# Kernel optimization log

Measured on AMD Instinct MI355X. Metric: run time of the kernel, lower is better.

Reference implementation:

```python
import jax, jax.numpy as jnp
import numpy as np

D_MODEL = 1024
N_HEADS = 16
HEAD_DIM = D_MODEL // N_HEADS  # 64; note: scores use full d_model dots but sqrt(head_dim) scale
WINDOW = 256
B, S = 4, 4096


def _window_starts(seq_len, ws):
    # replicate the torch loop: half-stride overlapping windows
    stride = ws // 2
    starts = []
    for i in range(0, seq_len, stride):
        end = min(i + ws, seq_len)
        start = max(0, end - ws)
        starts.append(start)
        if end == seq_len:
            break
    return np.asarray(starts, dtype=np.int32)


def setup_inputs() -> dict:
    key = jax.random.key(0)
    ks = jax.random.split(key, 9)
    sc = 0.02
    x = jax.random.normal(ks[0], (B, S, D_MODEL), dtype=jnp.float32)
    Wq = jax.random.normal(ks[1], (D_MODEL, D_MODEL), dtype=jnp.float32) * sc
    bq = jnp.zeros((D_MODEL,), jnp.float32)
    Wk = jax.random.normal(ks[2], (D_MODEL, D_MODEL), dtype=jnp.float32) * sc
    bk = jnp.zeros((D_MODEL,), jnp.float32)
    Wv = jax.random.normal(ks[3], (D_MODEL, D_MODEL), dtype=jnp.float32) * sc
    bv = jnp.zeros((D_MODEL,), jnp.float32)
    Wo = jax.random.normal(ks[4], (D_MODEL, D_MODEL), dtype=jnp.float32) * sc
    bo = jnp.zeros((D_MODEL,), jnp.float32)
    return {"x": x, "Wq": Wq, "bq": bq, "Wk": Wk, "bk": bk,
            "Wv": Wv, "bv": bv, "Wo": Wo, "bo": bo}


def reference(x, Wq, bq, Wk, bk, Wv, bv, Wo, bo):
    Bsz, seq, dm = x.shape
    q = x @ Wq + bq  # [B,S,D] (heads are re-flattened in the windowed path anyway)
    k = x @ Wk + bk
    v = x @ Wv + bv

    starts = _window_starts(seq, WINDOW)            # [W]
    idx = starts[:, None] + np.arange(WINDOW)[None]  # [W, ws] static indices
    idx_j = jnp.asarray(idx)

    qw = q[:, idx_j, :]  # [B, W, ws, D]
    kw = k[:, idx_j, :]
    vw = v[:, idx_j, :]

    scale = 1.0 / np.sqrt(HEAD_DIM).astype(np.float32)
    scores = jnp.einsum('bwid,bwjd->bwij', qw, kw) * scale  # full-d_model dots
    attn = jax.nn.softmax(scores, axis=-1)
    ow = jnp.einsum('bwij,bwjd->bwid', attn, vw)  # [B, W, ws, D]

    flat_idx = idx_j.reshape(-1)  # [W*ws]
    out = jnp.zeros_like(q).at[:, flat_idx, :].add(ow.reshape(Bsz, -1, dm))
    counts = jnp.zeros((seq,), jnp.float32).at[flat_idx].add(1.0)
    out = out / counts[None, :, None]  # overlap-add average

    return out @ Wo + bo
```

## Files before the change

### kernel.cpp

```cpp
#include <hip/hip_runtime.h>
#include <hip/hip_bf16.h>

typedef unsigned short u16;
typedef short bf16x8 __attribute__((ext_vector_type(8)));
typedef float f32x4 __attribute__((ext_vector_type(4)));
typedef float f32x16 __attribute__((ext_vector_type(16)));

#define DM     1024
#define SEQ    4096
#define NBATCH 4
#define NWIN   31
#define NTOK   16384

__device__ __forceinline__ u16 f2b(float f) {
  union { float f; unsigned u; } x; x.f = f;
  unsigned r = (x.u + 0x7fffu + ((x.u >> 16) & 1u)) >> 16;
  return (u16)r;
}
__device__ __forceinline__ float b2f(u16 v) {
  union { unsigned u; float f; } x; x.u = ((unsigned)v) << 16; return x.f;
}
__device__ __forceinline__ void gload_lds16(const u16* g, u16* l) {
  __builtin_amdgcn_global_load_lds(
      (const __attribute__((address_space(1))) void*)g,
      (__attribute__((address_space(3))) void*)l, 16, 0, 0);
}

__global__ __launch_bounds__(256) void k_convert(const float* __restrict__ in,
                                                 u16* __restrict__ out, int n4) {
  int i = blockIdx.x * 256 + threadIdx.x;
  if (i >= n4) return;
  float4 v = ((const float4*)in)[i];
  ushort4 o; o.x = f2b(v.x); o.y = f2b(v.y); o.z = f2b(v.z); o.w = f2b(v.w);
  ((ushort4*)out)[i] = o;
}

__global__ __launch_bounds__(256) void k_transpose4(const float* __restrict__ W0,
                                                    const float* __restrict__ W1,
                                                    const float* __restrict__ W2,
                                                    const float* __restrict__ W3,
                                                    u16* __restrict__ Wt) {
  __shared__ float tile[32][33];
  int z = blockIdx.z;
  const float* W = (z == 0) ? W0 : (z == 1) ? W1 : (z == 2) ? W2 : W3;
  u16* dst = Wt + (size_t)z * DM * DM;
  int n0 = blockIdx.x * 32, k0 = blockIdx.y * 32;
  int tx = threadIdx.x, ty = threadIdx.y;
  #pragma unroll
  for (int i = ty; i < 32; i += 8) tile[i][tx] = W[(size_t)(k0 + i) * DM + n0 + tx];
  __syncthreads();
  #pragma unroll
  for (int i = ty; i < 32; i += 8) dst[(size_t)(n0 + i) * DM + k0 + tx] = f2b(tile[tx][i]);
}

__global__ __launch_bounds__(256) void k_catbias(const float* __restrict__ bq,
                                                 const float* __restrict__ bk,
                                                 const float* __restrict__ bv,
                                                 float* __restrict__ o) {
  int i = blockIdx.x * 256 + threadIdx.x;
  if (i >= 3 * DM) return;
  float v = (i < DM) ? bq[i] : (i < 2 * DM) ? bk[i - DM] : bv[i - 2 * DM];
  o[i] = v;
}

__global__ __launch_bounds__(256, 4) void k_gemm(const u16* __restrict__ A, const u16* __restrict__ Bt,
                                                 const float* __restrict__ bias,
                                                 float* __restrict__ Cf,
                                                 u16* __restrict__ Cb, int ldc,
                                                 u16* __restrict__ Ct, int csplit,
                                                 int M, int N, int K) {
  __shared__ u16 As[128 * 64];
  __shared__ u16 Bs[128 * 64];
  const int tid = threadIdx.x;
  const int wv = tid >> 6, lane = tid & 63;
  const int l31 = lane & 31, hl = lane >> 5;
  const int lr8 = lane >> 3;
  const int lc8 = (((lane & 7) ^ (lr8 & 7)) * 8);
  const int m0 = blockIdx.y * 128, n0 = blockIdx.x * 128;
  const int wm = (wv >> 1) * 64, wn = (wv & 1) * 64;
  const int k7 = l31 & 7;
  f32x16 acc[2][2];
  #pragma unroll
  for (int a = 0; a < 2; ++a)
    #pragma unroll
    for (int b = 0; b < 2; ++b)
      #pragma unroll
      for (int r = 0; r < 16; ++r) acc[a][b][r] = 0.f;

  for (int kk = 0; kk < K; kk += 64) {
    #pragma unroll
    for (int j = 0; j < 4; ++j) {
      int e = wv * 4 + j;
      gload_lds16(A + (size_t)(m0 + e * 8 + lr8) * K + kk + lc8, As + e * 512);
    }
    #pragma unroll
    for (int j = 0; j < 4; ++j) {
      int e = wv * 4 + j;
      gload_lds16(Bt + (size_t)(n0 + e * 8 + lr8) * K + kk + lc8, Bs + e * 512);
    }
    __syncthreads();
    #pragma unroll
    for (int s = 0; s < 4; ++s) {
      const int ch = ((2 * s + hl) ^ k7) * 8;
      bf16x8 af[2], bfr[2];
      #pragma unroll
      for (int t = 0; t < 2; ++t) af[t]  = *(const bf16x8*)&As[(wm + t * 32 + l31) * 64 + ch];
      #pragma unroll
      for (int t = 0; t < 2; ++t) bfr[t] = *(const bf16x8*)&Bs[(wn + t * 32 + l31) * 64 + ch];
      #pragma unroll
      for (int mt = 0; mt < 2; ++mt)
        #pragma unroll
        for (int nt = 0; nt < 2; ++nt)
          acc[mt][nt] = __builtin_amdgcn_mfma_f32_32x32x16_bf16(af[mt], bfr[nt], acc[mt][nt], 0, 0, 0);
    }
    __syncthreads();
  }
  #pragma unroll
  for (int mt = 0; mt < 2; ++mt) {
    #pragma unroll
    for (int nt = 0; nt < 2; ++nt) {
      int col = n0 + wn + nt * 32 + l31;
      float bv = bias[col];
      #pragma unroll
      for (int g = 0; g < 4; ++g) {
        int row = m0 + wm + mt * 32 + g * 8 + hl * 4;
        if (Cf) {
          #pragma unroll
          for (int r = 0; r < 4; ++r)
            Cf[(size_t)(row + r) * N + col] = acc[mt][nt][g * 4 + r] + bv;
        } else if (col < csplit) {
          #pragma unroll
          for (int r = 0; r < 4; ++r)
            Cb[(size_t)(row + r) * ldc + col] = f2b(acc[mt][nt][g * 4 + r] + bv);
        } else {
          ushort4 o;
          o.x = f2b(acc[mt][nt][g * 4 + 0] + bv); o.y = f2b(acc[mt][nt][g * 4 + 1] + bv);
          o.z = f2b(acc[mt][nt][g * 4 + 2] + bv); o.w = f2b(acc[mt][nt][g * 4 + 3] + bv);
          *(ushort4*)&Ct[(size_t)(col - csplit) * M + row] = o;
        }
      }
    }
  }
}

#define PSTR 264
#define LDQ  2048
__global__ __launch_bounds__(256) void k_attn(const u16* __restrict__ QKb, const u16* __restrict__ Vt,
                                              u16* __restrict__ oA, u16* __restrict__ oB) {
  __shared__ u16 stage[10240];
  __shared__ u16 Pbuf[64 * PSTR];
  u16* Qs = stage;
  u16* Ks = stage + 2048;
  u16* Vs = stage;

  const int tid = threadIdx.x;
  const int wv = tid >> 6, lane = tid & 63;
  const int quad = lane >> 4, l16 = lane & 15;
  const int lr = lane >> 2;
  const int lc = (((lane & 3) ^ ((lr >> 1) & 3)) * 8);
  const int k3 = (l16 >> 1) & 3;
  const int qt = blockIdx.x >> 1, h = blockIdx.x & 1;
  const int w = blockIdx.y, b = blockIdx.z;
  const int s0 = w * 128;
  const size_t base2 = (size_t)b * SEQ * LDQ;
  const size_t base  = (size_t)b * SEQ * DM;
  const size_t btok  = (size_t)b * SEQ;
  const int qrow0 = s0 + qt * 64;

  f32x4 acc[16];
  #pragma unroll
  for (int i = 0; i < 16; ++i) acc[i] = (f32x4){0.f, 0.f, 0.f, 0.f};

  for (int kk = 0; kk < DM; kk += 32) {
    #pragma unroll
    for (int j = 0; j < 5; ++j) {
      int e = wv * 5 + j;
      if (e < 4) {
        gload_lds16(QKb + base2 + (size_t)(qrow0 + e * 16 + lr) * LDQ + kk + lc, Qs + e * 512);
      } else {
        int f = e - 4;
        gload_lds16(QKb + DM + base2 + (size_t)(s0 + f * 16 + lr) * LDQ + kk + lc, Ks + f * 512);
      }
    }
    __syncthreads();
    bf16x8 aq = *(const bf16x8*)&Qs[(wv * 16 + l16) * 32 + (quad ^ k3) * 8];
    #pragma unroll
    for (int nt = 0; nt < 16; ++nt) {
      bf16x8 bk = *(const bf16x8*)&Ks[(nt * 16 + l16) * 32 + (quad ^ k3) * 8];
      acc[nt] = __builtin_amdgcn_mfma_f32_16x16x32_bf16(aq, bk, acc[nt], 0, 0, 0);
    }
    __syncthreads();
  }

  float mx[4] = {-1e30f, -1e30f, -1e30f, -1e30f};
  float sm[4] = {0.f, 0.f, 0.f, 0.f};
  #pragma unroll
  for (int nt = 0; nt < 16; ++nt)
    #pragma unroll
    for (int r = 0; r < 4; ++r) {
      float s = acc[nt][r] * 0.125f;
      acc[nt][r] = s;
      mx[r] = fmaxf(mx[r], s);
    }
  #pragma unroll
  for (int r = 0; r < 4; ++r)
    #pragma unroll
    for (int off = 8; off > 0; off >>= 1)
      mx[r] = fmaxf(mx[r], __shfl_xor(mx[r], off, 64));
  #pragma unroll
  for (int nt = 0; nt < 16; ++nt)
    #pragma unroll
    for (int r = 0; r < 4; ++r) {
      float e = __expf(acc[nt][r] - mx[r]);
      acc[nt][r] = e;
      sm[r] += e;
    }
  #pragma unroll
  for (int r = 0; r < 4; ++r)
    #pragma unroll
    for (int off = 8; off > 0; off >>= 1)
      sm[r] += __shfl_xor(sm[r], off, 64);
  float inv[4];
  #pragma unroll
  for (int r = 0; r < 4; ++r) inv[r] = 1.f / sm[r];
  #pragma unroll
  for (int nt = 0; nt < 16; ++nt)
    #pragma unroll
    for (int r = 0; r < 4; ++r)
      Pbuf[(wv * 16 + quad * 4 + r) * PSTR + nt * 16 + l16] = f2b(acc[nt][r] * inv[r]);
  __syncthreads();

  u16* op = ((w & 1) ? oB : oA) + base;
  for (int sl = 0; sl < 2; ++sl) {
    const int nb = (h * 2 + sl) * 256;
    f32x4 acc2[4][4];
    #pragma unroll
    for (int a = 0; a < 4; ++a)
      #pragma unroll
      for (int c = 0; c < 4; ++c) acc2[a][c] = (f32x4){0.f, 0.f, 0.f, 0.f};
    for (int ks = 0; ks < 8; ++ks) {
      #pragma unroll
      for (int j = 0; j < 4; ++j) {
        int e = wv * 4 + j;
        gload_lds16(Vt + (size_t)(nb + e * 16 + lr) * NTOK + btok + s0 + ks * 32 + lc, Vs + e * 512);
      }
      __syncthreads();
      bf16x8 af[4];
      #pragma unroll
      for (int mt = 0; mt < 4; ++mt)
        af[mt] = *(const bf16x8*)&Pbuf[(mt * 16 + l16) * PSTR + ks * 32 + quad * 8];
      #pragma unroll
      for (int u = 0; u < 4; ++u) {
        bf16x8 bb = *(const bf16x8*)&Vs[((wv * 4 + u) * 16 + l16) * 32 + (quad ^ k3) * 8];
        #pragma unroll
        for (int mt = 0; mt < 4; ++mt)
          acc2[mt][u] = __builtin_amdgcn_mfma_f32_16x16x32_bf16(af[mt], bb, acc2[mt][u], 0, 0, 0);
      }
      __syncthreads();
    }
    #pragma unroll
    for (int mt = 0; mt < 4; ++mt)
      #pragma unroll
      for (int u = 0; u < 4; ++u) {
        int row = qrow0 + mt * 16 + quad * 4;
        int col = nb + (wv * 4 + u) * 16 + l16;
        #pragma unroll
        for (int r = 0; r < 4; ++r)
          op[(size_t)(row + r) * DM + col] = f2b(acc2[mt][u][r]);
      }
  }
}

__global__ __launch_bounds__(256) void k_norm(const u16* __restrict__ oA, const u16* __restrict__ oB,
                                              u16* __restrict__ out, int n8) {
  int i = blockIdx.x * 256 + threadIdx.x;
  if (i >= n8) return;
  int s = (i >> 7) & (SEQ - 1);
  uint4 a = ((const uint4*)oA)[i];
  uint4 r = a;
  if (s >= 128 && s < 3968) {
    uint4 bq = ((const uint4*)oB)[i];
    const unsigned* ap = (const unsigned*)&a;
    const unsigned* bp = (const unsigned*)&bq;
    unsigned* rp = (unsigned*)&r;
    #pragma unroll
    for (int k = 0; k < 4; ++k) {
      float lo = 0.5f * (b2f((u16)(ap[k] & 0xffff)) + b2f((u16)(bp[k] & 0xffff)));
      float hi = 0.5f * (b2f((u16)(ap[k] >> 16))    + b2f((u16)(bp[k] >> 16)));
      rp[k] = (unsigned)f2b(lo) | ((unsigned)f2b(hi) << 16);
    }
  }
  ((uint4*)out)[i] = r;
}

extern "C" void kernel_launch(void* const* d_in, const int* in_sizes, int n_in,
                              void* d_out, int out_size, void* d_ws, size_t ws_size,
                              hipStream_t stream) {
  const float* x  = (const float*)d_in[0];
  const float* Wq = (const float*)d_in[1];
  const float* bq = (const float*)d_in[2];
  const float* Wk = (const float*)d_in[3];
  const float* bk = (const float*)d_in[4];
  const float* Wv = (const float*)d_in[5];
  const float* bv = (const float*)d_in[6];
  const float* Wo = (const float*)d_in[7];
  const float* bo = (const float*)d_in[8];
  float* out = (float*)d_out;

  char* ws = (char*)d_ws;
  const size_t MB = 1024 * 1024;
  u16*   xb   = (u16*)(ws);
  u16*   qkb  = (u16*)(ws + 32 * MB);
  u16*   vtb  = (u16*)(ws + 96 * MB);
  u16*   wqt  = (u16*)(ws + 128 * MB);
  float* bcat = (float*)(ws + 136 * MB);
  u16*   oA   = (u16*)(ws + 137 * MB);
  u16*   oB   = (u16*)(ws + 169 * MB);

  int n4tok = (int)((size_t)NTOK * DM / 4);
  k_convert<<<(n4tok + 255) / 256, 256, 0, stream>>>(x, xb, n4tok);
  k_transpose4<<<dim3(DM / 32, DM / 32, 4), dim3(32, 8), 0, stream>>>(Wq, Wk, Wv, Wo, wqt);
  k_catbias<<<12, 256, 0, stream>>>(bq, bk, bv, bcat);

  k_gemm<<<dim3(3 * DM / 128, NTOK / 128), 256, 0, stream>>>(
      xb, wqt, bcat, nullptr, qkb, 2048, vtb, 2048, NTOK, 3 * DM, DM);

  k_attn<<<dim3(8, NWIN, NBATCH), 256, 0, stream>>>(qkb, vtb, oA, oB);

  int n8tok = (int)((size_t)NTOK * DM / 8);
  k_norm<<<(n8tok + 255) / 256, 256, 0, stream>>>(oA, oB, xb, n8tok);

  u16* wot = wqt + 3 * (size_t)DM * DM;
  k_gemm<<<dim3(DM / 128, NTOK / 128), 256, 0, stream>>>(
      xb, wot, bo, out, nullptr, DM, nullptr, DM, NTOK, DM, DM);
}
```

Baseline: 427.0 us.

## Restructure window attention tiling, add cross-wave softmax, swizzle LDS rows

The attention kernel now has each block own a 64-query tile against all 256 keys. Each wave holds a 64x64 score sub-tile, the K step is 64, and the softmax max and sum are reduced across waves through shared memory. This removes the earlier split where two blocks per query tile each recomputed the QK scores and covered only half the V columns. The launch changes to a flat 512-block grid with 2-blocks-per-SM bounds and a remapped block-to-(batch, window) order. LDS XOR swizzles are changed in both the GEMM and attention kernels to cut bank conflicts, at the cost of more LDS use per block and extra barriers.

```diff
diff --git a/kernel.cpp b/kernel.cpp
--- a/kernel.cpp
+++ b/kernel.cpp
@@ -74,11 +74,10 @@
   const int tid = threadIdx.x;
   const int wv = tid >> 6, lane = tid & 63;
   const int l31 = lane & 31, hl = lane >> 5;
-  const int lr8 = lane >> 3;
-  const int lc8 = (((lane & 7) ^ (lr8 & 7)) * 8);
+  const int l7 = lane & 7, lr8 = lane >> 3;
+  const int kq = (l31 & 7) + (l31 >> 3);
   const int m0 = blockIdx.y * 128, n0 = blockIdx.x * 128;
   const int wm = (wv >> 1) * 64, wn = (wv & 1) * 64;
-  const int k7 = l31 & 7;
   f32x16 acc[2][2];
   #pragma unroll
   for (int a = 0; a < 2; ++a)
@@ -91,22 +90,25 @@
     #pragma unroll
     for (int j = 0; j < 4; ++j) {
       int e = wv * 4 + j;
-      gload_lds16(A + (size_t)(m0 + e * 8 + lr8) * K + kk + lc8, As + e * 512);
+      int lc = (l7 ^ ((lr8 + e) & 7)) * 8;
+      gload_lds16(A + (size_t)(m0 + e * 8 + lr8) * K + kk + lc, As + e * 512);
     }
     #pragma unroll
     for (int j = 0; j < 4; ++j) {
       int e = wv * 4 + j;
-      gload_lds16(Bt + (size_t)(n0 + e * 8 + lr8) * K + kk + lc8, Bs + e * 512);
+      int lc = (l7 ^ ((lr8 + e) & 7)) * 8;
+      gload_lds16(Bt + (size_t)(n0 + e * 8 + lr8) * K + kk + lc, Bs + e * 512);
     }
     __syncthreads();
     #pragma unroll
     for (int s = 0; s < 4; ++s) {
-      const int ch = ((2 * s + hl) ^ k7) * 8;
       bf16x8 af[2], bfr[2];
       #pragma unroll
-      for (int t = 0; t < 2; ++t) af[t]  = *(const bf16x8*)&As[(wm + t * 32 + l31) * 64 + ch];
-      #pragma unroll
-      for (int t = 0; t < 2; ++t) bfr[t] = *(const bf16x8*)&Bs[(wn + t * 32 + l31) * 64 + ch];
+      for (int t = 0; t < 2; ++t)
+        af[t]  = *(const bf16x8*)&As[(wm + t * 32 + l31) * 64 + (((2 * s + hl) ^ ((kq + 4 * t) & 7)) * 8)];
+      #pragma unroll
+      for (int t = 0; t < 2; ++t)
+        bfr[t] = *(const bf16x8*)&Bs[(wn + t * 32 + l31) * 64 + (((2 * s + hl) ^ ((kq + 4 * t) & 7)) * 8)];
       #pragma unroll
       for (int mt = 0; mt < 2; ++mt)
         #pragma unroll
@@ -143,118 +145,186 @@
   }
 }
 
-#define PSTR 264
 #define LDQ  2048
-__global__ __launch_bounds__(256) void k_attn(const u16* __restrict__ QKb, const u16* __restrict__ Vt,
-                                              u16* __restrict__ oA, u16* __restrict__ oB) {
-  __shared__ u16 stage[10240];
-  __shared__ u16 Pbuf[64 * PSTR];
+__global__ __launch_bounds__(256, 2) void k_attn(const u16* __restrict__ QKb, const u16* __restrict__ Vt,
+                                                 u16* __restrict__ oA, u16* __restrict__ oB) {
+  __shared__ u16 stage[20480];
+  __shared__ u16 Pbuf[64 * 256];
+  __shared__ float red[2][4][64];
   u16* Qs = stage;
-  u16* Ks = stage + 2048;
+  u16* Ks = stage + 4096;
   u16* Vs = stage;
 
   const int tid = threadIdx.x;
   const int wv = tid >> 6, lane = tid & 63;
   const int quad = lane >> 4, l16 = lane & 15;
-  const int lr = lane >> 2;
-  const int lc = (((lane & 3) ^ ((lr >> 1) & 3)) * 8);
-  const int k3 = (l16 >> 1) & 3;
-  const int qt = blockIdx.x >> 1, h = blockIdx.x & 1;
-  const int w = blockIdx.y, b = blockIdx.z;
+  const int l7 = lane & 7, lr8 = lane >> 3;
+  const int kq = (l16 & 7) + (l16 >> 3);
+
+  int id = blockIdx.x;
+  int s_ = id >> 3;
+  int qt = s_ & 3;
+  int pair = (s_ >> 2) * 8 + (id & 7);
+  if (pair >= NWIN * NBATCH) return;
+  int b = pair / NWIN, w = pair - NWIN * b;
+
   const int s0 = w * 128;
   const size_t base2 = (size_t)b * SEQ * LDQ;
   const size_t base  = (size_t)b * SEQ * DM;
   const size_t btok  = (size_t)b * SEQ;
   const int qrow0 = s0 + qt * 64;
 
-  f32x4 acc[16];
-  #pragma unroll
-  for (int i = 0; i < 16; ++i) acc[i] = (f32x4){0.f, 0.f, 0.f, 0.f};
-
-  for (int kk = 0; kk < DM; kk += 32) {
-    #pragma unroll
-    for (int j = 0; j < 5; ++j) {
-      int e = wv * 5 + j;
-      if (e < 4) {
-        gload_lds16(QKb + base2 + (size_t)(qrow0 + e * 16 + lr) * LDQ + kk + lc, Qs + e * 512);
+  f32x4 acc[4][4];
+  #pragma unroll
+  for (int mt = 0; mt < 4; ++mt)
+    #pragma unroll
+    for (int nt = 0; nt < 4; ++nt) acc[mt][nt] = (f32x4){0.f, 0.f, 0.f, 0.f};
+
+  for (int kk = 0; kk < DM; kk += 64) {
+    #pragma unroll
+    for (int j = 0; j < 10; ++j) {
+      int idx = wv * 10 + j;
+      if (idx < 8) {
+        int lc = (l7 ^ ((lr8 + idx) & 7)) * 8;
+        gload_lds16(QKb + base2 + (size_t)(qrow0 + idx * 8 + lr8) * LDQ + kk + lc, Qs + idx * 512);
       } else {
-        int f = e - 4;
-        gload_lds16(QKb + DM + base2 + (size_t)(s0 + f * 16 + lr) * LDQ + kk + lc, Ks + f * 512);
+        int f = idx - 8;
+        int lc = (l7 ^ ((lr8 + f) & 7)) * 8;
+        gload_lds16(QKb + DM + base2 + (size_t)(s0 + f * 8 + lr8) * LDQ + kk + lc, Ks + f * 512);
       }
     }
     __syncthreads();
-    bf16x8 aq = *(const bf16x8*)&Qs[(wv * 16 + l16) * 32 + (quad ^ k3) * 8];
-    #pragma unroll
-    for (int nt = 0; nt < 16; ++nt) {
-      bf16x8 bk = *(const bf16x8*)&Ks[(nt * 16 + l16) * 32 + (quad ^ k3) * 8];
-      acc[nt] = __builtin_amdgcn_mfma_f32_16x16x32_bf16(aq, bk, acc[nt], 0, 0, 0);
+    #pragma unroll
+    for (int s2 = 0; s2 < 2; ++s2) {
+      bf16x8 aq[4], bk[4];
+      #pragma unroll
+      for (int mt = 0; mt < 4; ++mt)
+        aq[mt] = *(const bf16x8*)&Qs[(mt * 16 + l16) * 64 + (((s2 * 4 + quad) ^ ((kq + 2 * mt) & 7)) * 8)];
+      #pragma unroll
+      for (int nt = 0; nt < 4; ++nt)
+        bk[nt] = *(const bf16x8*)&Ks[(wv * 64 + nt * 16 + l16) * 64 + (((s2 * 4 + quad) ^ ((kq + 2 * nt) & 7)) * 8)];
+      #pragma unroll
+      for (int mt = 0; mt < 4; ++mt)
+        #pragma unroll
+        for (int nt = 0; nt < 4; ++nt)
+          acc[mt][nt] = __builtin_amdgcn_mfma_f32_16x16x32_bf16(aq[mt], bk[nt], acc[mt][nt], 0, 0, 0);
     }
     __syncthreads();
   }
 
-  float mx[4] = {-1e30f, -1e30f, -1e30f, -1e30f};
-  float sm[4] = {0.f, 0.f, 0.f, 0.f};
-  #pragma unroll
-  for (int nt = 0; nt < 16; ++nt)
+  float mx[4][4], sm[4][4];
+  #pragma unroll
+  for (int mt = 0; mt < 4; ++mt)
+    #pragma unroll
+    for (int r = 0; r < 4; ++r) mx[mt][r] = -1e30f;
+  #pragma unroll
+  for (int mt = 0; mt < 4; ++mt)
+    #pragma unroll
+    for (int nt = 0; nt < 4; ++nt)
+      #pragma unroll
+      for (int r = 0; r < 4; ++r) {
+        float v = acc[mt][nt][r] * 0.125f;
+        acc[mt][nt][r] = v;
+        mx[mt][r] = fmaxf(mx[mt][r], v);
+      }
+  #pragma unroll
+  for (int mt = 0; mt < 4; ++mt)
+    #pragma unroll
+    for (int r = 0; r < 4; ++r)
+      #pragma unroll
+      for (int off = 8; off > 0; off >>= 1)
+        mx[mt][r] = fmaxf(mx[mt][r], __shfl_xor(mx[mt][r], off, 64));
+  if (l16 == 0) {
+    #pragma unroll
+    for (int mt = 0; mt < 4; ++mt)
+      #pragma unroll
+      for (int r = 0; r < 4; ++r)
+        red[0][wv][mt * 16 + quad * 4 + r] = mx[mt][r];
+  }
+  __syncthreads();
+  float gm[4][4];
+  #pragma unroll
+  for (int mt = 0; mt < 4; ++mt)
     #pragma unroll
     for (int r = 0; r < 4; ++r) {
-      float s = acc[nt][r] * 0.125f;
-      acc[nt][r] = s;
-      mx[r] = fmaxf(mx[r], s);
-    }
-  #pragma unroll
-  for (int r = 0; r < 4; ++r)
-    #pragma unroll
-    for (int off = 8; off > 0; off >>= 1)
-      mx[r] = fmaxf(mx[r], __shfl_xor(mx[r], off, 64));
-  #pragma unroll
-  for (int nt = 0; nt < 16; ++nt)
+      int q = mt * 16 + quad * 4 + r;
+      gm[mt][r] = fmaxf(fmaxf(red[0][0][q], red[0][1][q]), fmaxf(red[0][2][q], red[0][3][q]));
+      sm[mt][r] = 0.f;
+    }
+  #pragma unroll
+  for (int mt = 0; mt < 4; ++mt)
+    #pragma unroll
+    for (int nt = 0; nt < 4; ++nt)
+      #pragma unroll
+      for (int r = 0; r < 4; ++r) {
+        float e = __expf(acc[mt][nt][r] - gm[mt][r]);
+        acc[mt][nt][r] = e;
+        sm[mt][r] += e;
+      }
+  #pragma unroll
+  for (int mt = 0; mt < 4; ++mt)
+    #pragma unroll
+    for (int r = 0; r < 4; ++r)
+      #pragma unroll
+      for (int off = 8; off > 0; off >>= 1)
+        sm[mt][r] += __shfl_xor(sm[mt][r], off, 64);
+  if (l16 == 0) {
+    #pragma unroll
+    for (int mt = 0; mt < 4; ++mt)
+      #pragma unroll
+      for (int r = 0; r < 4; ++r)
+        red[1][wv][mt * 16 + quad * 4 + r] = sm[mt][r];
+  }
+  __syncthreads();
+  #pragma unroll
+  for (int mt = 0; mt < 4; ++mt)
     #pragma unroll
     for (int r = 0; r < 4; ++r) {
-      float e = __expf(acc[nt][r] - mx[r]);
-      acc[nt][r] = e;
-      sm[r] += e;
-    }
-  #pragma unroll
-  for (int r = 0; r < 4; ++r)
-    #pragma unroll
-    for (int off = 8; off > 0; off >>= 1)
-      sm[r] += __shfl_xor(sm[r], off, 64);
-  float inv[4];
-  #pragma unroll
-  for (int r = 0; r < 4; ++r) inv[r] = 1.f / sm[r];
-  #pragma unroll
-  for (int nt = 0; nt < 16; ++nt)
-    #pragma unroll
-    for (int r = 0; r < 4; ++r)
-      Pbuf[(wv * 16 + quad * 4 + r) * PSTR + nt * 16 + l16] = f2b(acc[nt][r] * inv[r]);
+      int q = mt * 16 + quad * 4 + r;
+      float inv = 1.f / (red[1][0][q] + red[1][1][q] + red[1][2][q] + red[1][3][q]);
+      #pragma unroll
+      for (int nt = 0; nt < 4; ++nt) {
+        int ke = wv * 64 + nt * 16 + l16;
+        int phys = (ke >> 3) ^ (q & 7);
+        Pbuf[q * 256 + phys * 8 + (ke & 7)] = f2b(acc[mt][nt][r] * inv);
+      }
+    }
   __syncthreads();
 
   u16* op = ((w & 1) ? oB : oA) + base;
-  for (int sl = 0; sl < 2; ++sl) {
-    const int nb = (h * 2 + sl) * 256;
+  for (int slab = 0; slab < 4; ++slab) {
+    const int nb = slab * 256;
     f32x4 acc2[4][4];
     #pragma unroll
-    for (int a = 0; a < 4; ++a)
-      #pragma unroll
-      for (int c = 0; c < 4; ++c) acc2[a][c] = (f32x4){0.f, 0.f, 0.f, 0.f};
-    for (int ks = 0; ks < 8; ++ks) {
-      #pragma unroll
-      for (int j = 0; j < 4; ++j) {
-        int e = wv * 4 + j;
-        gload_lds16(Vt + (size_t)(nb + e * 16 + lr) * NTOK + btok + s0 + ks * 32 + lc, Vs + e * 512);
+    for (int mt = 0; mt < 4; ++mt)
+      #pragma unroll
+      for (int u = 0; u < 4; ++u) acc2[mt][u] = (f32x4){0.f, 0.f, 0.f, 0.f};
+    for (int sk = 0; sk < 4; ++sk) {
+      const int tok0 = sk * 64;
+      #pragma unroll
+      for (int j = 0; j < 8; ++j) {
+        int e = wv * 8 + j;
+        int lc = (l7 ^ ((lr8 + e) & 7)) * 8;
+        gload_lds16(Vt + (size_t)(nb + e * 8 + lr8) * NTOK + btok + s0 + tok0 + lc, Vs + e * 512);
       }
       __syncthreads();
-      bf16x8 af[4];
-      #pragma unroll
-      for (int mt = 0; mt < 4; ++mt)
-        af[mt] = *(const bf16x8*)&Pbuf[(mt * 16 + l16) * PSTR + ks * 32 + quad * 8];
-      #pragma unroll
-      for (int u = 0; u < 4; ++u) {
-        bf16x8 bb = *(const bf16x8*)&Vs[((wv * 4 + u) * 16 + l16) * 32 + (quad ^ k3) * 8];
+      #pragma unroll
+      for (int s2 = 0; s2 < 2; ++s2) {
+        bf16x8 af[4];
         #pragma unroll
-        for (int mt = 0; mt < 4; ++mt)
-          acc2[mt][u] = __builtin_amdgcn_mfma_f32_16x16x32_bf16(af[mt], bb, acc2[mt][u], 0, 0, 0);
+        for (int mt = 0; mt < 4; ++mt) {
+          int cP = sk * 8 + s2 * 4 + quad;
+          int phys = cP ^ (l16 & 7);
+          af[mt] = *(const bf16x8*)&Pbuf[(mt * 16 + l16) * 256 + phys * 8];
+        }
+        #pragma unroll
+        for (int u = 0; u < 4; ++u) {
+          bf16x8 bb = *(const bf16x8*)&Vs[(wv * 64 + u * 16 + l16) * 64 +
+                                          (((s2 * 4 + quad) ^ ((kq + 2 * u) & 7)) * 8)];
+          #pragma unroll
+          for (int mt = 0; mt < 4; ++mt)
+            acc2[mt][u] = __builtin_amdgcn_mfma_f32_16x16x32_bf16(af[mt], bb, acc2[mt][u], 0, 0, 0);
+        }
       }
       __syncthreads();
     }
@@ -263,7 +333,7 @@
       #pragma unroll
       for (int u = 0; u < 4; ++u) {
         int row = qrow0 + mt * 16 + quad * 4;
-        int col = nb + (wv * 4 + u) * 16 + l16;
+        int col = nb + wv * 64 + u * 16 + l16;
         #pragma unroll
         for (int r = 0; r < 4; ++r)
           op[(size_t)(row + r) * DM + col] = f2b(acc2[mt][u][r]);
@@ -325,7 +395,7 @@
   k_gemm<<<dim3(3 * DM / 128, NTOK / 128), 256, 0, stream>>>(
       xb, wqt, bcat, nullptr, qkb, 2048, vtb, 2048, NTOK, 3 * DM, DM);
 
-  k_attn<<<dim3(8, NWIN, NBATCH), 256, 0, stream>>>(qkb, vtb, oA, oB);
+  k_attn<<<512, 256, 0, stream>>>(qkb, vtb, oA, oB);
 
   int n8tok = (int)((size_t)NTOK * DM / 8);
   k_norm<<<(n8tok + 255) / 256, 256, 0, stream>>>(oA, oB, xb, n8tok);
```

Result: faster. 376.9 us (-11.7%).
